# Kernel optimization log

Measured on AMD Instinct MI355X. Metric: run time of the kernel, lower is better.

The kernel has to match this reference:

```python
import jax, jax.numpy as jnp
import numpy as np

N = 100000      # nodes
K = 32          # fixed neighbor degree
DIN = 256
DOUT = 128


def setup_inputs() -> dict:
    key = jax.random.key(0)
    k1, k2, k3, k4 = jax.random.split(key, 4)
    feats = jax.random.normal(k1, (N, DIN), dtype=jnp.float32)
    edge_dict = jax.random.randint(k2, (N, K), 0, N, dtype=jnp.int32)
    W = jax.random.normal(k3, (DIN, DOUT), dtype=jnp.float32) * (1.0 / np.sqrt(DIN))
    b = jax.random.normal(k4, (DOUT,), dtype=jnp.float32) * 0.01
    return {"feats": feats, "edge_dict": edge_dict, "W": W, "b": b}


def reference(feats, edge_dict, W, b):
    # fc -> relu (dropout is identity in eval mode)
    h = jax.nn.relu(feats @ W + b)                 # [N, DOUT]
    # per-node neighbor gather + mean (ragged loop in torch -> one fused gather)
    pooled = jnp.mean(h[edge_dict], axis=1)        # [N, K, DOUT] -> [N, DOUT]
    return pooled
```

## Files before the change

kernel.cpp:

```cpp
#include <hip/hip_runtime.h>
#include <hip/hip_bf16.h>

#define NN   100000
#define KNB  32
#define DIN  256
#define DOUT 128

typedef __attribute__((ext_vector_type(8))) short short8;
typedef __attribute__((ext_vector_type(4))) float f32x4;
typedef __attribute__((ext_vector_type(4))) unsigned u32x4;
typedef __attribute__((ext_vector_type(2))) int i32x2;

__device__ __forceinline__ unsigned pk2(float a, float b) {
    unsigned r;
    asm("v_cvt_pk_bf16_f32 %0, %1, %2" : "=v"(r) : "v"(a), "v"(b));
    return r;
}

__device__ __forceinline__ short8 cvt8(f32x4 a, f32x4 b) {
    u32x4 t;
    t[0] = pk2(a[0], a[1]);
    t[1] = pk2(a[2], a[3]);
    t[2] = pk2(b[0], b[1]);
    t[3] = pk2(b[2], b[3]);
    return __builtin_bit_cast(short8, t);
}

__device__ __forceinline__ void load_lds16(const float* g, float* l) {
    __builtin_amdgcn_global_load_lds(
        (const __attribute__((address_space(1))) void*)g,
        (__attribute__((address_space(3))) void*)l, 16, 0, 0);
}

__global__ void wt_conv(const float* __restrict__ W, unsigned short* __restrict__ Wt) {
    int t = blockIdx.x * 256 + threadIdx.x;
    int d = t >> 8;
    int k = t & 255;
    float v = W[(size_t)k * DOUT + d];
    Wt[t] = (unsigned short)(pk2(v, v) & 0xffffu);
}

__global__ __launch_bounds__(256, 4) void gemm_relu(
        const float* __restrict__ feats, const unsigned short* __restrict__ Wt,
        const float* __restrict__ bias, unsigned short* __restrict__ h) {
    __shared__ float sf[32 * DIN];

    const int tid  = threadIdx.x;
    const int lane = tid & 63;
    const int w    = tid >> 6;
    const int l16  = lane & 15;
    const int lq   = lane >> 4;
    const int blockBase = blockIdx.x * 32;

    short8 afrag[2][8];
    const unsigned short* wp = Wt + (size_t)(w * 32 + l16) * DIN + lq * 8;
    #pragma unroll
    for (int m = 0; m < 2; ++m)
        #pragma unroll
        for (int ks = 0; ks < 8; ++ks)
            afrag[m][ks] = *(const short8*)(wp + m * 16 * DIN + ks * 32);

    #pragma unroll
    for (int it = 0; it < 8; ++it) {
        int row = it * 4 + w;
        int cd  = lane;
        int cs  = cd ^ (row & 7);
        load_lds16(feats + (size_t)(blockBase + row) * DIN + cs * 4,
                   sf + it * 1024 + tid * 4);
    }

    asm volatile("s_waitcnt vmcnt(0)" ::: "memory");
    __syncthreads();

    f32x4 acc[2][2];
    acc[0][0] = (f32x4)0.f; acc[0][1] = (f32x4)0.f;
    acc[1][0] = (f32x4)0.f; acc[1][1] = (f32x4)0.f;

    #pragma unroll
    for (int ks = 0; ks < 8; ++ks) {
        short8 bf0, bf1;
        {
            const float* rbase = sf + (size_t)l16 * DIN;
            f32x4 x0 = *(const f32x4*)(rbase + ((ks * 8 + 2 * lq)     ^ (l16 & 7)) * 4);
            f32x4 x1 = *(const f32x4*)(rbase + ((ks * 8 + 2 * lq + 1) ^ (l16 & 7)) * 4);
            bf0 = cvt8(x0, x1);
        }
        {
            const float* rbase = sf + (size_t)(16 + l16) * DIN;
            f32x4 x0 = *(const f32x4*)(rbase + ((ks * 8 + 2 * lq)     ^ (l16 & 7)) * 4);
            f32x4 x1 = *(const f32x4*)(rbase + ((ks * 8 + 2 * lq + 1) ^ (l16 & 7)) * 4);
            bf1 = cvt8(x0, x1);
        }
        #pragma unroll
        for (int m = 0; m < 2; ++m) {
            acc[m][0] = __builtin_amdgcn_mfma_f32_16x16x32_bf16(afrag[m][ks], bf0, acc[m][0], 0, 0, 0);
            acc[m][1] = __builtin_amdgcn_mfma_f32_16x16x32_bf16(afrag[m][ks], bf1, acc[m][1], 0, 0, 0);
        }
    }

    #pragma unroll
    for (int m = 0; m < 2; ++m) {
        int dbase = w * 32 + m * 16 + lq * 4;
        f32x4 bv = *(const f32x4*)(bias + dbase);
        #pragma unroll
        for (int nf = 0; nf < 2; ++nf) {
            int node = blockBase + nf * 16 + l16;
            f32x4 v = acc[m][nf];
            float v0 = fmaxf(v[0] + bv[0], 0.f);
            float v1 = fmaxf(v[1] + bv[1], 0.f);
            float v2 = fmaxf(v[2] + bv[2], 0.f);
            float v3 = fmaxf(v[3] + bv[3], 0.f);
            uint2 st = make_uint2(pk2(v0, v1), pk2(v2, v3));
            *(uint2*)(h + (size_t)node * DOUT + dbase) = st;
        }
    }
}

__global__ __launch_bounds__(256) void gather_mean(
        const int* __restrict__ edge, const unsigned short* __restrict__ h,
        float* __restrict__ out, int nbase) {
    const int q = threadIdx.x & 15;
    const int n = nbase + blockIdx.x * 16 + (threadIdx.x >> 4);

    i32x2 e2 = __builtin_nontemporal_load((const i32x2*)(edge + (size_t)n * KNB + q * 2));

    float s0=0,s1=0,s2=0,s3=0,s4=0,s5=0,s6=0,s7=0;

    #define ROW(k) ((size_t)((k) < 16 ? __shfl(e2[0], (k), 16) \
                                      : __shfl(e2[1], (k) - 16, 16)) * DOUT)
    #define LD(k)  (*(const u32x4*)(h + ROW(k) + q * 8))
    #define ACC(v) do { \
        s0 += __uint_as_float((v)[0] << 16); \
        s1 += __uint_as_float((v)[0] & 0xffff0000u); \
        s2 += __uint_as_float((v)[1] << 16); \
        s3 += __uint_as_float((v)[1] & 0xffff0000u); \
        s4 += __uint_as_float((v)[2] << 16); \
        s5 += __uint_as_float((v)[2] & 0xffff0000u); \
        s6 += __uint_as_float((v)[3] << 16); \
        s7 += __uint_as_float((v)[3] & 0xffff0000u); } while (0)
    #define STEP(k, B) do { u32x4 v_ = (B); \
        if ((k) + 8 < KNB) (B) = LD((k) + 8); \
        ACC(v_); } while (0)

    u32x4 b0 = LD(0), b1 = LD(1), b2 = LD(2), b3 = LD(3);
    u32x4 b4 = LD(4), b5 = LD(5), b6 = LD(6), b7 = LD(7);

    STEP( 0, b0); STEP( 1, b1); STEP( 2, b2); STEP( 3, b3);
    STEP( 4, b4); STEP( 5, b5); STEP( 6, b6); STEP( 7, b7);
    STEP( 8, b0); STEP( 9, b1); STEP(10, b2); STEP(11, b3);
    STEP(12, b4); STEP(13, b5); STEP(14, b6); STEP(15, b7);
    STEP(16, b0); STEP(17, b1); STEP(18, b2); STEP(19, b3);
    STEP(20, b4); STEP(21, b5); STEP(22, b6); STEP(23, b7);
    STEP(24, b0); STEP(25, b1); STEP(26, b2); STEP(27, b3);
    STEP(28, b4); STEP(29, b5); STEP(30, b6); STEP(31, b7);

    #undef STEP
    #undef ACC
    #undef LD
    #undef ROW

    const float sc = 1.f / KNB;
    f32x4 o0 = { s0 * sc, s1 * sc, s2 * sc, s3 * sc };
    f32x4 o1 = { s4 * sc, s5 * sc, s6 * sc, s7 * sc };
    float* op = out + (size_t)n * DOUT + q * 8;
    __builtin_nontemporal_store(o0, (f32x4*)op);
    __builtin_nontemporal_store(o1, (f32x4*)(op + 4));
}

extern "C" void kernel_launch(void* const* d_in, const int* in_sizes, int n_in,
                              void* d_out, int out_size, void* d_ws, size_t ws_size,
                              hipStream_t stream) {
    const float* feats = (const float*)d_in[0];
    const int*   edge  = (const int*)d_in[1];
    const float* W     = (const float*)d_in[2];
    const float* b     = (const float*)d_in[3];
    float* out = (float*)d_out;

    unsigned short* Wt = (unsigned short*)d_ws;
    unsigned short* h  = (unsigned short*)((char*)d_ws + 65536);

    wt_conv<<<128, 256, 0, stream>>>(W, Wt);
    gemm_relu<<<NN / 32, 256, 0, stream>>>(feats, Wt, b, h);
    gather_mean<<<(NN / 2) / 16, 256, 0, stream>>>(edge, h, out, 0);
    gather_mean<<<(NN / 2) / 16, 256, 0, stream>>>(edge, h, out, NN / 2);
}
```

Before: 151.8 us.

## Gather neighbors in node-range chunks so each pass hits cache

Replaces the per-node gather with a kernel where each block handles 80 nodes and sweeps ten source-node ranges. In each sweep it only loads neighbor rows whose index falls in the current 10000-node range. The goal is to keep the working set of h small enough to stay in L2/MALL and avoid random DRAM traffic. In exchange every neighbor index is tested ten times with divergent branches, and loads are serialised behind those branches, so latency hiding may suffer.

Measured after the change: 293.7 us. 1.93x slower.

```diff
diff --git a/kernel.cpp b/kernel.cpp
--- a/kernel.cpp
+++ b/kernel.cpp
@@ -5,6 +5,8 @@
 #define KNB  32
 #define DIN  256
 #define DOUT 128
+#define CHUNKN 10000
+#define NCHUNK 10
 
 typedef __attribute__((ext_vector_type(8))) short short8;
 typedef __attribute__((ext_vector_type(4))) float f32x4;
@@ -116,55 +118,83 @@
     }
 }
 
-__global__ __launch_bounds__(256) void gather_mean(
+__global__ __launch_bounds__(256) void gather_chunked(
         const int* __restrict__ edge, const unsigned short* __restrict__ h,
-        float* __restrict__ out, int nbase) {
+        float* __restrict__ out) {
     const int q = threadIdx.x & 15;
-    const int n = nbase + blockIdx.x * 16 + (threadIdx.x >> 4);
-
-    i32x2 e2 = __builtin_nontemporal_load((const i32x2*)(edge + (size_t)n * KNB + q * 2));
-
-    float s0=0,s1=0,s2=0,s3=0,s4=0,s5=0,s6=0,s7=0;
-
-    #define ROW(k) ((size_t)((k) < 16 ? __shfl(e2[0], (k), 16) \
-                                      : __shfl(e2[1], (k) - 16, 16)) * DOUT)
-    #define LD(k)  (*(const u32x4*)(h + ROW(k) + q * 8))
-    #define ACC(v) do { \
-        s0 += __uint_as_float((v)[0] << 16); \
-        s1 += __uint_as_float((v)[0] & 0xffff0000u); \
-        s2 += __uint_as_float((v)[1] << 16); \
-        s3 += __uint_as_float((v)[1] & 0xffff0000u); \
-        s4 += __uint_as_float((v)[2] << 16); \
-        s5 += __uint_as_float((v)[2] & 0xffff0000u); \
-        s6 += __uint_as_float((v)[3] << 16); \
-        s7 += __uint_as_float((v)[3] & 0xffff0000u); } while (0)
-    #define STEP(k, B) do { u32x4 v_ = (B); \
-        if ((k) + 8 < KNB) (B) = LD((k) + 8); \
-        ACC(v_); } while (0)
-
-    u32x4 b0 = LD(0), b1 = LD(1), b2 = LD(2), b3 = LD(3);
-    u32x4 b4 = LD(4), b5 = LD(5), b6 = LD(6), b7 = LD(7);
-
-    STEP( 0, b0); STEP( 1, b1); STEP( 2, b2); STEP( 3, b3);
-    STEP( 4, b4); STEP( 5, b5); STEP( 6, b6); STEP( 7, b7);
-    STEP( 8, b0); STEP( 9, b1); STEP(10, b2); STEP(11, b3);
-    STEP(12, b4); STEP(13, b5); STEP(14, b6); STEP(15, b7);
-    STEP(16, b0); STEP(17, b1); STEP(18, b2); STEP(19, b3);
-    STEP(20, b4); STEP(21, b5); STEP(22, b6); STEP(23, b7);
-    STEP(24, b0); STEP(25, b1); STEP(26, b2); STEP(27, b3);
-    STEP(28, b4); STEP(29, b5); STEP(30, b6); STEP(31, b7);
-
-    #undef STEP
-    #undef ACC
-    #undef LD
-    #undef ROW
+    const int g = threadIdx.x >> 4;
+    const int nodeBase = blockIdx.x * 80;
+
+    i32x2 e0 = *(const i32x2*)(edge + (size_t)(nodeBase +  0 + g) * KNB + q * 2);
+    i32x2 e1 = *(const i32x2*)(edge + (size_t)(nodeBase + 16 + g) * KNB + q * 2);
+    i32x2 e2 = *(const i32x2*)(edge + (size_t)(nodeBase + 32 + g) * KNB + q * 2);
+    i32x2 e3 = *(const i32x2*)(edge + (size_t)(nodeBase + 48 + g) * KNB + q * 2);
+    i32x2 e4 = *(const i32x2*)(edge + (size_t)(nodeBase + 64 + g) * KNB + q * 2);
+
+    f32x4 lo0 = (f32x4)0.f, hi0 = (f32x4)0.f;
+    f32x4 lo1 = (f32x4)0.f, hi1 = (f32x4)0.f;
+    f32x4 lo2 = (f32x4)0.f, hi2 = (f32x4)0.f;
+    f32x4 lo3 = (f32x4)0.f, hi3 = (f32x4)0.f;
+    f32x4 lo4 = (f32x4)0.f, hi4 = (f32x4)0.f;
+
+    #define KEEP(E) do { int a_ = (E)[0], b_ = (E)[1]; \
+        asm volatile("" : "+v"(a_), "+v"(b_)); (E)[0] = a_; (E)[1] = b_; } while (0)
+
+    #define GK(k, EE, LO, HI) do { \
+        int e_ = ((k) < 16) ? __shfl((EE)[0], (k), 16) \
+                            : __shfl((EE)[1], (k) - 16, 16); \
+        if ((unsigned)(e_ - clo) < (unsigned)CHUNKN) { \
+            u32x4 v_ = *(const u32x4*)(h + (size_t)e_ * DOUT + q * 8); \
+            LO[0] += __uint_as_float(v_[0] << 16); \
+            LO[1] += __uint_as_float(v_[0] & 0xffff0000u); \
+            LO[2] += __uint_as_float(v_[1] << 16); \
+            LO[3] += __uint_as_float(v_[1] & 0xffff0000u); \
+            HI[0] += __uint_as_float(v_[2] << 16); \
+            HI[1] += __uint_as_float(v_[2] & 0xffff0000u); \
+            HI[2] += __uint_as_float(v_[3] << 16); \
+            HI[3] += __uint_as_float(v_[3] & 0xffff0000u); \
+        } } while (0)
+
+    #define BATCH32(EE, LO, HI) do { \
+        GK( 0, EE, LO, HI); GK( 1, EE, LO, HI); GK( 2, EE, LO, HI); GK( 3, EE, LO, HI); \
+        GK( 4, EE, LO, HI); GK( 5, EE, LO, HI); GK( 6, EE, LO, HI); GK( 7, EE, LO, HI); \
+        GK( 8, EE, LO, HI); GK( 9, EE, LO, HI); GK(10, EE, LO, HI); GK(11, EE, LO, HI); \
+        GK(12, EE, LO, HI); GK(13, EE, LO, HI); GK(14, EE, LO, HI); GK(15, EE, LO, HI); \
+        GK(16, EE, LO, HI); GK(17, EE, LO, HI); GK(18, EE, LO, HI); GK(19, EE, LO, HI); \
+        GK(20, EE, LO, HI); GK(21, EE, LO, HI); GK(22, EE, LO, HI); GK(23, EE, LO, HI); \
+        GK(24, EE, LO, HI); GK(25, EE, LO, HI); GK(26, EE, LO, HI); GK(27, EE, LO, HI); \
+        GK(28, EE, LO, HI); GK(29, EE, LO, HI); GK(30, EE, LO, HI); GK(31, EE, LO, HI); \
+    } while (0)
+
+    #pragma unroll 1
+    for (int c = 0; c < NCHUNK; ++c) {
+        const int clo = c * CHUNKN;
+        KEEP(e0); KEEP(e1); KEEP(e2); KEEP(e3); KEEP(e4);
+        BATCH32(e0, lo0, hi0);
+        BATCH32(e1, lo1, hi1);
+        BATCH32(e2, lo2, hi2);
+        BATCH32(e3, lo3, hi3);
+        BATCH32(e4, lo4, hi4);
+    }
+
+    #undef BATCH32
+    #undef GK
+    #undef KEEP
 
     const float sc = 1.f / KNB;
-    f32x4 o0 = { s0 * sc, s1 * sc, s2 * sc, s3 * sc };
-    f32x4 o1 = { s4 * sc, s5 * sc, s6 * sc, s7 * sc };
-    float* op = out + (size_t)n * DOUT + q * 8;
-    __builtin_nontemporal_store(o0, (f32x4*)op);
-    __builtin_nontemporal_store(o1, (f32x4*)(op + 4));
+    #define STORE(B, LO, HI) do { \
+        float* op_ = out + (size_t)(nodeBase + (B) * 16 + g) * DOUT + q * 8; \
+        f32x4 o0_ = { LO[0] * sc, LO[1] * sc, LO[2] * sc, LO[3] * sc }; \
+        f32x4 o1_ = { HI[0] * sc, HI[1] * sc, HI[2] * sc, HI[3] * sc }; \
+        __builtin_nontemporal_store(o0_, (f32x4*)op_); \
+        __builtin_nontemporal_store(o1_, (f32x4*)(op_ + 4)); } while (0)
+
+    STORE(0, lo0, hi0);
+    STORE(1, lo1, hi1);
+    STORE(2, lo2, hi2);
+    STORE(3, lo3, hi3);
+    STORE(4, lo4, hi4);
+    #undef STORE
 }
 
 extern "C" void kernel_launch(void* const* d_in, const int* in_sizes, int n_in,
@@ -181,6 +211,5 @@
 
     wt_conv<<<128, 256, 0, stream>>>(W, Wt);
     gemm_relu<<<NN / 32, 256, 0, stream>>>(feats, Wt, b, h);
-    gather_mean<<<(NN / 2) / 16, 256, 0, stream>>>(edge, h, out, 0);
-    gather_mean<<<(NN / 2) / 16, 256, 0, stream>>>(edge, h, out, NN / 2);
-}
+    gather_chunked<<<NN / 80, 256, 0, stream>>>(edge, h, out);
+}
```

## Bucket neighbor indices by row chunk to improve gather cache locality

Applied to the files above, without the earlier changes.

Adds a pre-pass that counting-sorts each node's 32 neighbor indices into 10 chunks of the h table and stores per-node chunk offsets. A new gather kernel handles 80 nodes per block and walks the chunks in lockstep, so concurrent loads hit a narrow slice of h and stay in L2. The cost is an extra kernel that reads edge_dict and writes a sorted copy plus offsets, and a gather with data-dependent loops, no prefetch pipelining and fewer blocks. If the workspace is too small it falls back to a single-launch gather_mean.

New measurement: 232.1 us. +52.9%, slower.

```diff
diff --git a/kernel.cpp b/kernel.cpp
--- a/kernel.cpp
+++ b/kernel.cpp
@@ -5,10 +5,13 @@
 #define KNB  32
 #define DIN  256
 #define DOUT 128
+#define CHUNKN 10000
+#define NCHUNK 10
 
 typedef __attribute__((ext_vector_type(8))) short short8;
 typedef __attribute__((ext_vector_type(4))) float f32x4;
 typedef __attribute__((ext_vector_type(4))) unsigned u32x4;
+typedef __attribute__((ext_vector_type(4))) int i32x4;
 typedef __attribute__((ext_vector_type(2))) int i32x2;
 
 __device__ __forceinline__ unsigned pk2(float a, float b) {
@@ -31,6 +34,8 @@
         (const __attribute__((address_space(1))) void*)g,
         (__attribute__((address_space(3))) void*)l, 16, 0, 0);
 }
+
+#define CHUNKOF(e) __umulhi((unsigned)(e), 429497u)
 
 __global__ void wt_conv(const float* __restrict__ W, unsigned short* __restrict__ Wt) {
     int t = blockIdx.x * 256 + threadIdx.x;
@@ -116,11 +121,109 @@
     }
 }
 
+__global__ __launch_bounds__(256) void edge_sort(
+        const int* __restrict__ edge, int* __restrict__ sorted,
+        unsigned long long* __restrict__ pfx) {
+    int n = blockIdx.x * 256 + threadIdx.x;
+    if (n >= NN) return;
+    const i32x4* ep = (const i32x4*)(edge + (size_t)n * KNB);
+    i32x4 E0 = ep[0], E1 = ep[1], E2 = ep[2], E3 = ep[3];
+    i32x4 E4 = ep[4], E5 = ep[5], E6 = ep[6], E7 = ep[7];
+
+    unsigned long long cnt = 0;
+    #define CNT1(e) (cnt += 1ULL << (6 * CHUNKOF(e)))
+    #define CNT4(E) do { CNT1((E)[0]); CNT1((E)[1]); CNT1((E)[2]); CNT1((E)[3]); } while (0)
+    CNT4(E0); CNT4(E1); CNT4(E2); CNT4(E3); CNT4(E4); CNT4(E5); CNT4(E6); CNT4(E7);
+    #undef CNT4
+    #undef CNT1
+
+    unsigned long long off = 0;
+    unsigned run = 0;
+    #pragma unroll
+    for (int c = 0; c < NCHUNK; ++c) {
+        off |= (unsigned long long)run << (6 * c);
+        run += (unsigned)((cnt >> (6 * c)) & 63ULL);
+    }
+    pfx[n] = off;
+
+    int* sp = sorted + (size_t)n * KNB;
+    #define PUT1(e) do { unsigned c_ = CHUNKOF(e); \
+        sp[(unsigned)((off >> (6 * c_)) & 63ULL)] = (e); \
+        off += 1ULL << (6 * c_); } while (0)
+    #define PUT4(E) do { PUT1((E)[0]); PUT1((E)[1]); PUT1((E)[2]); PUT1((E)[3]); } while (0)
+    PUT4(E0); PUT4(E1); PUT4(E2); PUT4(E3); PUT4(E4); PUT4(E5); PUT4(E6); PUT4(E7);
+    #undef PUT4
+    #undef PUT1
+}
+
+__global__ __launch_bounds__(256) void gather_sorted(
+        const int* __restrict__ sorted, const unsigned long long* __restrict__ pfx,
+        const unsigned short* __restrict__ h, float* __restrict__ out) {
+    const int q = threadIdx.x & 15;
+    const int g = threadIdx.x >> 4;
+    const int nodeBase = blockIdx.x * 80;
+
+    const int n0 = nodeBase + g;
+    unsigned long long p0 = pfx[n0];
+    unsigned long long p1 = pfx[n0 + 16];
+    unsigned long long p2 = pfx[n0 + 32];
+    unsigned long long p3 = pfx[n0 + 48];
+    unsigned long long p4 = pfx[n0 + 64];
+
+    f32x4 lo0 = (f32x4)0.f, hi0 = (f32x4)0.f;
+    f32x4 lo1 = (f32x4)0.f, hi1 = (f32x4)0.f;
+    f32x4 lo2 = (f32x4)0.f, hi2 = (f32x4)0.f;
+    f32x4 lo3 = (f32x4)0.f, hi3 = (f32x4)0.f;
+    f32x4 lo4 = (f32x4)0.f, hi4 = (f32x4)0.f;
+
+    #define RUNB(NODE, P, LO, HI) do { \
+        int st_ = (int)((P >> (6 * c)) & 63ULL); \
+        int en_ = (c < NCHUNK - 1) ? (int)((P >> (6 * c + 6)) & 63ULL) : KNB; \
+        const int* sp_ = sorted + (size_t)(NODE) * KNB; \
+        for (int j = st_; j < en_; ++j) { \
+            int e_ = sp_[j]; \
+            u32x4 v_ = *(const u32x4*)(h + (size_t)e_ * DOUT + q * 8); \
+            LO[0] += __uint_as_float(v_[0] << 16); \
+            LO[1] += __uint_as_float(v_[0] & 0xffff0000u); \
+            LO[2] += __uint_as_float(v_[1] << 16); \
+            LO[3] += __uint_as_float(v_[1] & 0xffff0000u); \
+            HI[0] += __uint_as_float(v_[2] << 16); \
+            HI[1] += __uint_as_float(v_[2] & 0xffff0000u); \
+            HI[2] += __uint_as_float(v_[3] << 16); \
+            HI[3] += __uint_as_float(v_[3] & 0xffff0000u); \
+        } } while (0)
+
+    #pragma unroll 1
+    for (int c = 0; c < NCHUNK; ++c) {
+        RUNB(n0,      p0, lo0, hi0);
+        RUNB(n0 + 16, p1, lo1, hi1);
+        RUNB(n0 + 32, p2, lo2, hi2);
+        RUNB(n0 + 48, p3, lo3, hi3);
+        RUNB(n0 + 64, p4, lo4, hi4);
+    }
+    #undef RUNB
+
+    const float sc = 1.f / KNB;
+    #define STORE(B, LO, HI) do { \
+        float* op_ = out + (size_t)(nodeBase + (B) * 16 + g) * DOUT + q * 8; \
+        f32x4 o0_ = { LO[0] * sc, LO[1] * sc, LO[2] * sc, LO[3] * sc }; \
+        f32x4 o1_ = { HI[0] * sc, HI[1] * sc, HI[2] * sc, HI[3] * sc }; \
+        __builtin_nontemporal_store(o0_, (f32x4*)op_); \
+        __builtin_nontemporal_store(o1_, (f32x4*)(op_ + 4)); } while (0)
+
+    STORE(0, lo0, hi0);
+    STORE(1, lo1, hi1);
+    STORE(2, lo2, hi2);
+    STORE(3, lo3, hi3);
+    STORE(4, lo4, hi4);
+    #undef STORE
+}
+
 __global__ __launch_bounds__(256) void gather_mean(
         const int* __restrict__ edge, const unsigned short* __restrict__ h,
-        float* __restrict__ out, int nbase) {
+        float* __restrict__ out) {
     const int q = threadIdx.x & 15;
-    const int n = nbase + blockIdx.x * 16 + (threadIdx.x >> 4);
+    const int n = blockIdx.x * 16 + (threadIdx.x >> 4);
 
     i32x2 e2 = __builtin_nontemporal_load((const i32x2*)(edge + (size_t)n * KNB + q * 2));
 
@@ -178,9 +281,19 @@
 
     unsigned short* Wt = (unsigned short*)d_ws;
     unsigned short* h  = (unsigned short*)((char*)d_ws + 65536);
+    const size_t sortedOff = 65536 + (size_t)NN * DOUT * 2;
+    const size_t pfxOff    = sortedOff + (size_t)NN * KNB * 4;
+    const size_t need      = pfxOff + (size_t)NN * 8;
 
     wt_conv<<<128, 256, 0, stream>>>(W, Wt);
     gemm_relu<<<NN / 32, 256, 0, stream>>>(feats, Wt, b, h);
-    gather_mean<<<(NN / 2) / 16, 256, 0, stream>>>(edge, h, out, 0);
-    gather_mean<<<(NN / 2) / 16, 256, 0, stream>>>(edge, h, out, NN / 2);
-}
+
+    if (ws_size >= need) {
+        int* sorted = (int*)((char*)d_ws + sortedOff);
+        unsigned long long* pfx = (unsigned long long*)((char*)d_ws + pfxOff);
+        edge_sort<<<(NN + 255) / 256, 256, 0, stream>>>(edge, sorted, pfx);
+        gather_sorted<<<NN / 80, 256, 0, stream>>>(sorted, pfx, h, out);
+    } else {
+        gather_mean<<<NN / 16, 256, 0, stream>>>(edge, h, out);
+    }
+}
```

## Make GEMM persistent with double-buffered LDS prefetch and merge gather launches

Applied to the files above, without the earlier changes.

The GEMM kernel becomes persistent over a fixed grid of 512 blocks. Each block loops over 32-row tiles and prefetches the next tile into a second LDS buffer while computing the current one. This spreads the cost of loading W fragments and bias across many tiles and overlaps global-to-LDS traffic with MFMA work. The two gather launches are merged into one, saving a launch. The larger LDS footprint lowers occupancy to 2 blocks, and 512 blocks may not fill every CU evenly.

Result: faster. 138.4 us (-8.8%).

```diff
diff --git a/kernel.cpp b/kernel.cpp
--- a/kernel.cpp
+++ b/kernel.cpp
@@ -5,6 +5,8 @@
 #define KNB  32
 #define DIN  256
 #define DOUT 128
+#define NT   (NN / 32)
+#define GEMM_GRID 512
 
 typedef __attribute__((ext_vector_type(8))) short short8;
 typedef __attribute__((ext_vector_type(4))) float f32x4;
@@ -40,17 +42,16 @@
     Wt[t] = (unsigned short)(pk2(v, v) & 0xffffu);
 }
 
-__global__ __launch_bounds__(256, 4) void gemm_relu(
+__global__ __launch_bounds__(256, 2) void gemm_relu(
         const float* __restrict__ feats, const unsigned short* __restrict__ Wt,
         const float* __restrict__ bias, unsigned short* __restrict__ h) {
-    __shared__ float sf[32 * DIN];
+    __shared__ float sbuf[2][32 * DIN];
 
     const int tid  = threadIdx.x;
     const int lane = tid & 63;
     const int w    = tid >> 6;
     const int l16  = lane & 15;
     const int lq   = lane >> 4;
-    const int blockBase = blockIdx.x * 32;
 
     short8 afrag[2][8];
     const unsigned short* wp = Wt + (size_t)(w * 32 + l16) * DIN + lq * 8;
@@ -60,67 +61,88 @@
         for (int ks = 0; ks < 8; ++ks)
             afrag[m][ks] = *(const short8*)(wp + m * 16 * DIN + ks * 32);
 
-    #pragma unroll
-    for (int it = 0; it < 8; ++it) {
-        int row = it * 4 + w;
-        int cd  = lane;
-        int cs  = cd ^ (row & 7);
-        load_lds16(feats + (size_t)(blockBase + row) * DIN + cs * 4,
-                   sf + it * 1024 + tid * 4);
-    }
-
-    asm volatile("s_waitcnt vmcnt(0)" ::: "memory");
-    __syncthreads();
-
-    f32x4 acc[2][2];
-    acc[0][0] = (f32x4)0.f; acc[0][1] = (f32x4)0.f;
-    acc[1][0] = (f32x4)0.f; acc[1][1] = (f32x4)0.f;
-
-    #pragma unroll
-    for (int ks = 0; ks < 8; ++ks) {
-        short8 bf0, bf1;
-        {
-            const float* rbase = sf + (size_t)l16 * DIN;
-            f32x4 x0 = *(const f32x4*)(rbase + ((ks * 8 + 2 * lq)     ^ (l16 & 7)) * 4);
-            f32x4 x1 = *(const f32x4*)(rbase + ((ks * 8 + 2 * lq + 1) ^ (l16 & 7)) * 4);
-            bf0 = cvt8(x0, x1);
-        }
-        {
-            const float* rbase = sf + (size_t)(16 + l16) * DIN;
-            f32x4 x0 = *(const f32x4*)(rbase + ((ks * 8 + 2 * lq)     ^ (l16 & 7)) * 4);
-            f32x4 x1 = *(const f32x4*)(rbase + ((ks * 8 + 2 * lq + 1) ^ (l16 & 7)) * 4);
-            bf1 = cvt8(x0, x1);
-        }
+    f32x4 bv0 = *(const f32x4*)(bias + w * 32 + lq * 4);
+    f32x4 bv1 = *(const f32x4*)(bias + w * 32 + 16 + lq * 4);
+
+    auto stage = [&](int tile, int pb) {
+        #pragma unroll
+        for (int it = 0; it < 8; ++it) {
+            int row = it * 4 + w;
+            int cs  = lane ^ (row & 7);
+            load_lds16(feats + (size_t)(tile * 32 + row) * DIN + cs * 4,
+                       &sbuf[pb][it * 1024 + tid * 4]);
+        }
+    };
+
+    int t  = blockIdx.x;
+    if (t >= NT) return;
+    stage(t, 0);
+    int pb = 0;
+
+    for (; t < NT; t += GEMM_GRID) {
+        int tn = t + GEMM_GRID;
+        if (tn < NT) {
+            stage(tn, pb ^ 1);
+            asm volatile("s_waitcnt vmcnt(8)" ::: "memory");
+        } else {
+            asm volatile("s_waitcnt vmcnt(0)" ::: "memory");
+        }
+        __syncthreads();
+
+        f32x4 acc[2][2];
+        acc[0][0] = (f32x4)0.f; acc[0][1] = (f32x4)0.f;
+        acc[1][0] = (f32x4)0.f; acc[1][1] = (f32x4)0.f;
+
+        const float* buf = sbuf[pb];
+        #pragma unroll
+        for (int ks = 0; ks < 8; ++ks) {
+            short8 bf0, bf1;
+            {
+                const float* rbase = buf + (size_t)l16 * DIN;
+                f32x4 x0 = *(const f32x4*)(rbase + ((ks * 8 + 2 * lq)     ^ (l16 & 7)) * 4);
+                f32x4 x1 = *(const f32x4*)(rbase + ((ks * 8 + 2 * lq + 1) ^ (l16 & 7)) * 4);
+                bf0 = cvt8(x0, x1);
+            }
+            {
+                const float* rbase = buf + (size_t)(16 + l16) * DIN;
+                f32x4 x0 = *(const f32x4*)(rbase + ((ks * 8 + 2 * lq)     ^ (l16 & 7)) * 4);
+                f32x4 x1 = *(const f32x4*)(rbase + ((ks * 8 + 2 * lq + 1) ^ (l16 & 7)) * 4);
+                bf1 = cvt8(x0, x1);
+            }
+            #pragma unroll
+            for (int m = 0; m < 2; ++m) {
+                acc[m][0] = __builtin_amdgcn_mfma_f32_16x16x32_bf16(afrag[m][ks], bf0, acc[m][0], 0, 0, 0);
+                acc[m][1] = __builtin_amdgcn_mfma_f32_16x16x32_bf16(afrag[m][ks], bf1, acc[m][1], 0, 0, 0);
+            }
+        }
+
         #pragma unroll
         for (int m = 0; m < 2; ++m) {
-            acc[m][0] = __builtin_amdgcn_mfma_f32_16x16x32_bf16(afrag[m][ks], bf0, acc[m][0], 0, 0, 0);
-            acc[m][1] = __builtin_amdgcn_mfma_f32_16x16x32_bf16(afrag[m][ks], bf1, acc[m][1], 0, 0, 0);
-        }
-    }
-
-    #pragma unroll
-    for (int m = 0; m < 2; ++m) {
-        int dbase = w * 32 + m * 16 + lq * 4;
-        f32x4 bv = *(const f32x4*)(bias + dbase);
-        #pragma unroll
-        for (int nf = 0; nf < 2; ++nf) {
-            int node = blockBase + nf * 16 + l16;
-            f32x4 v = acc[m][nf];
-            float v0 = fmaxf(v[0] + bv[0], 0.f);
-            float v1 = fmaxf(v[1] + bv[1], 0.f);
-            float v2 = fmaxf(v[2] + bv[2], 0.f);
-            float v3 = fmaxf(v[3] + bv[3], 0.f);
-            uint2 st = make_uint2(pk2(v0, v1), pk2(v2, v3));
-            *(uint2*)(h + (size_t)node * DOUT + dbase) = st;
-        }
+            int dbase = w * 32 + m * 16 + lq * 4;
+            f32x4 bv = (m == 0) ? bv0 : bv1;
+            #pragma unroll
+            for (int nf = 0; nf < 2; ++nf) {
+                int node = t * 32 + nf * 16 + l16;
+                f32x4 v = acc[m][nf];
+                float v0 = fmaxf(v[0] + bv[0], 0.f);
+                float v1 = fmaxf(v[1] + bv[1], 0.f);
+                float v2 = fmaxf(v[2] + bv[2], 0.f);
+                float v3 = fmaxf(v[3] + bv[3], 0.f);
+                uint2 st = make_uint2(pk2(v0, v1), pk2(v2, v3));
+                *(uint2*)(h + (size_t)node * DOUT + dbase) = st;
+            }
+        }
+
+        __syncthreads();
+        pb ^= 1;
     }
 }
 
 __global__ __launch_bounds__(256) void gather_mean(
         const int* __restrict__ edge, const unsigned short* __restrict__ h,
-        float* __restrict__ out, int nbase) {
+        float* __restrict__ out) {
     const int q = threadIdx.x & 15;
-    const int n = nbase + blockIdx.x * 16 + (threadIdx.x >> 4);
+    const int n = blockIdx.x * 16 + (threadIdx.x >> 4);
 
     i32x2 e2 = __builtin_nontemporal_load((const i32x2*)(edge + (size_t)n * KNB + q * 2));
 
@@ -180,7 +202,6 @@
     unsigned short* h  = (unsigned short*)((char*)d_ws + 65536);
 
     wt_conv<<<128, 256, 0, stream>>>(W, Wt);
-    gemm_relu<<<NN / 32, 256, 0, stream>>>(feats, Wt, b, h);
-    gather_mean<<<(NN / 2) / 16, 256, 0, stream>>>(edge, h, out, 0);
-    gather_mean<<<(NN / 2) / 16, 256, 0, stream>>>(edge, h, out, NN / 2);
-}
+    gemm_relu<<<GEMM_GRID, 256, 0, stream>>>(feats, Wt, b, h);
+    gather_mean<<<NN / 16, 256, 0, stream>>>(edge, h, out);
+}
```
